# Kernel optimization log

Hardware: AMD Instinct MI355X
Metric: run time of the kernel (lower is better)

Reference implementation:

```python
import jax, jax.numpy as jnp
import numpy as np

DIM = 256
CDIM = 512
HEADS = 8
DIM_HEAD = 32
HID = HEADS * DIM_HEAD          # 256
MLP_DIM = int(DIM * 2.5)        # 640
B, T, TC = 8, 8192, 8192
GROUPS = 32
EPS = 1e-5


def setup_inputs() -> dict:
    key = jax.random.key(0)
    ks = jax.random.split(key, 12)
    w = lambda k, shape: jax.random.normal(k, shape, jnp.float32) * 0.02
    return {
        "x": jax.random.normal(ks[0], (B, DIM, T), jnp.float32),
        "c": jax.random.normal(ks[1], (B, CDIM, TC), jnp.float32),
        # self-attn (LinearAttention)
        "W_qkv": w(ks[2], (3 * HID, DIM)),
        "W_so": w(ks[3], (DIM, HID)), "b_so": jnp.zeros((DIM,), jnp.float32),
        "sa_g": jnp.ones((DIM,), jnp.float32), "sa_b": jnp.zeros((DIM,), jnp.float32),
        # cross-attn (LinearAttentionC)
        "W_cq": w(ks[4], (HID, DIM)),
        "W_ckv": w(ks[5], (2 * HID, CDIM)),
        "W_co": w(ks[6], (DIM, HID)), "b_co": jnp.zeros((DIM,), jnp.float32),
        "ca_g": jnp.ones((DIM,), jnp.float32), "ca_b": jnp.zeros((DIM,), jnp.float32),
        # MLP
        "W_m1": w(ks[7], (MLP_DIM, DIM)), "b_m1": jnp.zeros((MLP_DIM,), jnp.float32),
        "W_m2": w(ks[8], (DIM, MLP_DIM)), "b_m2": jnp.zeros((DIM,), jnp.float32),
        # pre-norms
        "nm_g": jnp.ones((DIM,), jnp.float32), "nm_b": jnp.zeros((DIM,), jnp.float32),
        "nm1_g": jnp.ones((DIM,), jnp.float32), "nm1_b": jnp.zeros((DIM,), jnp.float32),
        "nm2_g": jnp.ones((DIM,), jnp.float32), "nm2_b": jnp.zeros((DIM,), jnp.float32),
        "nm3_g": jnp.ones((CDIM,), jnp.float32), "nm3_b": jnp.zeros((CDIM,), jnp.float32),
    }


def group_norm(x, g, b):
    Bx, C, Tx = x.shape
    xg = x.reshape(Bx, GROUPS, C // GROUPS, Tx)
    mu = xg.mean(axis=(2, 3), keepdims=True)
    var = ((xg - mu) ** 2).mean(axis=(2, 3), keepdims=True)
    xn = ((xg - mu) * jax.lax.rsqrt(var + EPS)).reshape(Bx, C, Tx)
    return xn * g[None, :, None] + b[None, :, None]


def conv1(x, W, b=None):
    # 1x1 Conv1d == channel matmul: W [out, in], x [b, in, t]
    y = jnp.einsum('oc,bct->bot', W, x)
    return y if b is None else y + b[None, :, None]


def split_heads(t):
    Bx, HC, Tx = t.shape
    return t.reshape(Bx, HEADS, HC // HEADS, Tx)  # b h c t


def linear_attention(q, k, v):
    # q,k,v: [b, h, d, t]
    scale = DIM_HEAD ** -0.5
    q = jax.nn.softmax(q, axis=-2) * scale   # softmax over feature dim d
    k = jax.nn.softmax(k, axis=-1)           # softmax over time t
    ctx = jnp.einsum('bhdn,bhen->bhde', k, v)   # [b,h,d,e] tiny per-head context
    out = jnp.einsum('bhde,bhdn->bhen', ctx, q)
    Bx, H, E, Tx = out.shape
    return out.reshape(Bx, H * E, Tx)  # b (h c) t


def reference(x, c, W_qkv, W_so, b_so, sa_g, sa_b,
              W_cq, W_ckv, W_co, b_co, ca_g, ca_b,
              W_m1, b_m1, W_m2, b_m2,
              nm_g, nm_b, nm1_g, nm1_b, nm2_g, nm2_b, nm3_g, nm3_b):
    # --- self linear attention + residual ---
    h = group_norm(x, nm_g, nm_b)
    q, k, v = map(split_heads, jnp.split(conv1(h, W_qkv), 3, axis=1))
    o = linear_attention(q, k, v)
    o = group_norm(conv1(o, W_so, b_so), sa_g, sa_b)
    x = o + x
    # --- cross linear attention + residual ---
    h = group_norm(x, nm1_g, nm1_b)
    cn = group_norm(c, nm3_g, nm3_b)
    q = split_heads(conv1(h, W_cq))
    k, v = map(split_heads, jnp.split(conv1(cn, W_ckv), 2, axis=1))
    o = linear_attention(q, k, v)
    o = group_norm(conv1(o, W_co, b_co), ca_g, ca_b)
    x = o + x
    # --- SiLU MLP + residual ---
    h = group_norm(x, nm2_g, nm2_b)
    h = jax.nn.silu(conv1(h, W_m1, b_m1))
    x = conv1(h, W_m2, b_m2) + x
    return x
```

## Files before the change

kernel.cpp:

```cpp
#include <hip/hip_runtime.h>
#include <cmath>

typedef unsigned short u16;
typedef __attribute__((ext_vector_type(8))) __bf16 bf16x8;
typedef __attribute__((ext_vector_type(4))) float f32x4;

#define DEV static __device__ __forceinline__

DEV float b2f(u16 u){ union{unsigned i; float f;} v; v.i=((unsigned)u)<<16; return v.f; }
DEV u16 f2b(float f){ union{float f; unsigned i;} v; v.f=f; unsigned r = v.i + 0x7FFFu + ((v.i>>16)&1u); return (u16)(r>>16); }

#define GLL(g,l) __builtin_amdgcn_global_load_lds((const __attribute__((address_space(1))) void*)(g), (__attribute__((address_space(3))) void*)(l), 16, 0, 0)

__global__ void k_init(const float* __restrict__ s0,const float* __restrict__ s1,
                       const float* __restrict__ s2, u16* __restrict__ d,
                       float* __restrict__ stats){
  const int bid = blockIdx.x;
  if (bid == 1152){
    #pragma unroll
    for (int j=0;j<12;j++){ const int idx=j*256+threadIdx.x; if (idx<3072) stats[idx]=0.f; }
    return;
  }
  const int i = bid*256 + threadIdx.x;
  const float* s; int off;
  if      (i < 65536){ s=s0; off=0; }
  else if (i < 131072){ s=s1; off=65536; }
  else                { s=s2; off=131072; }
  d[i] = f2b(s[i-off]);
}

DEV void fold_body(const float* W, const float* g, const float* beta, const float* base,
                   const float* stats, u16* Wb, float* biasb, int O, int K, int chsh,
                   float inv_n, int o, int b){
  const int tid = threadIdx.x;
  float bp = 0.f;
  for (int k = tid; k < K; k += 256){
    const int gr = k >> chsh;
    const float s = stats[(b*32+gr)*2], s2 = stats[(b*32+gr)*2+1];
    const float mu = s*inv_n;
    const float rs = rsqrtf(s2*inv_n - mu*mu + 1e-5f);
    const float w = W[(long)o*K + k];
    const float gg = g[k]*rs;
    Wb[((long)b*O + o)*K + k] = f2b(w*gg);
    bp += w*(beta[k] - mu*gg);
  }
  __shared__ float red[256];
  red[tid] = bp; __syncthreads();
  for (int off=128; off>0; off>>=1){ if (tid<off) red[tid]+=red[tid+off]; __syncthreads(); }
  if (tid==0) biasb[b*O+o] = red[0] + (base ? base[o] : 0.f);
}

__global__ void k_fold(const float* __restrict__ W, const float* __restrict__ g,
                       const float* __restrict__ beta, const float* __restrict__ base,
                       const float* __restrict__ stats, u16* __restrict__ Wb,
                       float* __restrict__ biasb, int O, int K, int chsh, float inv_n){
  fold_body(W,g,beta,base,stats,Wb,biasb,O,K,chsh,inv_n,blockIdx.x,blockIdx.y);
}

__global__ void k_fold2(const float* __restrict__ W1, const float* __restrict__ g1,
                        const float* __restrict__ be1, const float* __restrict__ st1,
                        u16* __restrict__ Wb1, float* __restrict__ bb1, int O1, int K1, int chsh1, float inv1,
                        const float* __restrict__ W2, const float* __restrict__ g2,
                        const float* __restrict__ be2, const float* __restrict__ st2,
                        u16* __restrict__ Wb2, float* __restrict__ bb2, int O2, int K2, int chsh2, float inv2){
  const int o = blockIdx.x, b = blockIdx.y;
  if (o < O1) fold_body(W1,g1,be1,nullptr,st1,Wb1,bb1,O1,K1,chsh1,inv1,o,b);
  else        fold_body(W2,g2,be2,nullptr,st2,Wb2,bb2,O2,K2,chsh2,inv2,o-O1,b);
}

__global__ void k_transs(const float* __restrict__ xsrc, const float* __restrict__ csrc,
                         u16* __restrict__ xdst, u16* __restrict__ cdst,
                         float* __restrict__ xstat, float* __restrict__ cstat){
  const int b = blockIdx.z;
  const int gy = blockIdx.y;
  const float* src; u16* dst; float* stat; int C, chsh, c0;
  if (gy < 4){ src=xsrc; dst=xdst; stat=xstat; C=256; chsh=3; c0=gy*64; }
  else       { src=csrc; dst=cdst; stat=cstat; C=512; chsh=4; c0=(gy-4)*64; }
  const int t0 = blockIdx.x*64;
  const int tid = threadIdx.x;
  __shared__ float tile[64][65];
  __shared__ float grp[16];
  if (tid < 16) grp[tid] = 0.f;
  float s_acc[4], s2_acc[4];
  #pragma unroll
  for (int p=0;p<4;p++){
    const int cc = (tid>>4) + p*16, tt = (tid&15)*4;
    const float4 v = *(const float4*)&src[((long)b*C + c0+cc)*8192 + t0+tt];
    tile[cc][tt+0]=v.x; tile[cc][tt+1]=v.y; tile[cc][tt+2]=v.z; tile[cc][tt+3]=v.w;
    s_acc[p]  = v.x+v.y+v.z+v.w;
    s2_acc[p] = v.x*v.x+v.y*v.y+v.z*v.z+v.w*v.w;
  }
  __syncthreads();
  #pragma unroll
  for (int p=0;p<4;p++){
    float s = s_acc[p], s2 = s2_acc[p];
    #pragma unroll
    for (int m=1; m<16; m<<=1){ s += __shfl_xor(s, m); s2 += __shfl_xor(s2, m); }
    if ((tid&15)==0){
      const int gl = ((tid>>4) + p*16) >> chsh;
      atomicAdd(&grp[gl*2],   s);
      atomicAdd(&grp[gl*2+1], s2);
    }
  }
  #pragma unroll
  for (int p=0;p<4;p++){
    const int tt = (tid>>4) + p*16, c4 = (tid&15)*4;
    u16 rbi[4];
    #pragma unroll
    for (int j=0;j<4;j++) rbi[j] = f2b(tile[c4+j][tt]);
    ushort4 rv; rv.x=rbi[0]; rv.y=rbi[1]; rv.z=rbi[2]; rv.w=rbi[3];
    *(ushort4*)&dst[((long)b*8192 + t0+tt)*C + c0+c4] = rv;
  }
  __syncthreads();
  const int ngr = 64>>chsh;
  if (tid < ngr*2){
    atomicAdd(&stat[((b*32) + (c0>>chsh))*2 + tid], grp[tid]);
  }
}

template<bool OUTB, bool BIAS, bool SILU, bool RES, bool STATS, bool SPLIT, bool TRANS>
__global__ __launch_bounds__(256,2) void k_gemm(
    const u16* __restrict__ A, const u16* __restrict__ W,
    float* __restrict__ outF, u16* __restrict__ outB,
    const float* __restrict__ bias, const u16* __restrict__ res,
    float* __restrict__ stat, int K, int O, long wsb, int bsb)
{
  __shared__ u16 As[128*64];
  __shared__ u16 Ws[128*64];
  __shared__ float sb[128][2];
  const int tid = threadIdx.x;
  const int wv = tid>>6, lane = tid&63;
  const int nwg = (int)(gridDim.x*gridDim.y);
  int fid = (int)(blockIdx.y*gridDim.x + blockIdx.x);
  fid = (fid&7)*(nwg>>3) + (fid>>3);
  const long t0 = (long)(fid / (int)gridDim.x)*128;
  const int o0 = (fid % (int)gridDim.x)*128;
  const int bb = (int)(t0>>13);
  const u16* Wp = W + (long)bb*wsb;
  const int wt = (wv>>1)*64, wo = (wv&1)*64;
  const int lr = lane>>3, lc = (lane&7)*8;
  f32x4 acc[4][4] = {};
  for (int kc = 0; kc < K; kc += 64){
    #pragma unroll
    for (int it = 0; it < 4; ++it){
      const int r = wv*32 + it*8;
      GLL(A + (t0 + r + lr)*(long)K + kc + lc, &As[r*64]);
      GLL(Wp + (long)(o0 + r + lr)*K + kc + lc, &Ws[r*64]);
    }
    __syncthreads();
    #pragma unroll
    for (int ks=0; ks<2; ++ks){
      const int kb = ks*32 + (lane>>4)*8;
      bf16x8 af[4], bfr[4];
      #pragma unroll
      for (int i=0;i<4;i++) af[i]  = *(const bf16x8*)&As[(wt + i*16 + (lane&15))*64 + kb];
      #pragma unroll
      for (int j=0;j<4;j++) bfr[j] = *(const bf16x8*)&Ws[(wo + j*16 + (lane&15))*64 + kb];
      #pragma unroll
      for (int i=0;i<4;i++)
        #pragma unroll
        for (int j=0;j<4;j++)
          acc[i][j] = __builtin_amdgcn_mfma_f32_16x16x32_bf16(af[i], bfr[j], acc[i][j], 0, 0, 0);
    }
    __syncthreads();
  }
  if (STATS){
    if (tid < 128){ sb[tid][0]=0.f; sb[tid][1]=0.f; }
    __syncthreads();
  }
  const int q = lane>>4, cc = lane&15;
  #pragma unroll
  for (int j=0;j<4;j++){
    const int o = o0 + wo + j*16 + cc;
    const float bv = BIAS ? bias[bsb*bb + o] : 0.f;
    float ts=0.f, ts2=0.f;
    #pragma unroll
    for (int i=0;i<4;i++){
      const long tb = t0 + wt + i*16 + q*4;
      if (TRANS){
        float vv[4];
        #pragma unroll
        for (int r=0;r<4;r++){
          float v = acc[i][j][r] + bv;
          if (SILU) v = v * (1.f/(1.f + __expf(-v)));
          if (RES) v += b2f(res[(tb + r)*(long)O + o]);
          vv[r] = v;
        }
        float4 v4; v4.x=vv[0]; v4.y=vv[1]; v4.z=vv[2]; v4.w=vv[3];
        *(float4*)&outF[(((tb>>13)*(long)O + o)<<13) + (tb&8191)] = v4;
      } else {
        #pragma unroll
        for (int r=0;r<4;r++){
          float v = acc[i][j][r] + bv;
          if (SILU) v = v * (1.f/(1.f + __expf(-v)));
          long idx;
          if (SPLIT) idx = ((long)(o>>8)<<24) + (tb + r)*256 + (o&255);
          else       idx = (tb + r)*(long)O + o;
          if (RES) v += b2f(res[idx]);
          if (STATS){ ts += v; ts2 += v*v; }
          if (OUTB) outB[idx] = f2b(v); else outF[idx] = v;
        }
      }
    }
    if (STATS){
      const int ol = wo + j*16 + cc;
      atomicAdd(&sb[ol][0], ts);
      atomicAdd(&sb[ol][1], ts2);
    }
  }
  if (STATS){
    __syncthreads();
    if (tid < 16){
      float u=0.f, u2=0.f;
      #pragma unroll
      for (int j2=0;j2<8;j2++){ u += sb[tid*8+j2][0]; u2 += sb[tid*8+j2][1]; }
      atomicAdd(&stat[(bb*32 + (o0>>3) + tid)*2],   u);
      atomicAdd(&stat[(bb*32 + (o0>>3) + tid)*2+1], u2);
    }
  }
}

__global__ __launch_bounds__(256,2) void k_ctx(const u16* __restrict__ kp, const u16* __restrict__ vp,
                                               float* __restrict__ part){
  const int tid = threadIdx.x;
  const int b = blockIdx.x >> 6, seg = blockIdx.x & 63;
  const int h = tid>>5, d = tid&31;
  __shared__ u16 kb[16][256];
  __shared__ float vf[16][260];
  float acc[32];
  #pragma unroll
  for (int e=0;e<32;e++) acc[e]=0.f;
  float ks = 0.f;
  const long rb = (long)b*8192 + seg*128;
  const int w = tid>>6, sub = tid&63;
  for (int tc=0; tc<128; tc+=16){
    #pragma unroll
    for (int p=0;p<4;p++){
      const int row = p*4 + w;
      const long rowbase = (rb + tc + row)*256;
      if (sub < 32){
        uint4 val = *(const uint4*)(kp + rowbase + sub*8);
        *(uint4*)&kb[row][sub*8] = val;
      } else {
        const int s2 = sub-32;
        uint4 val = *(const uint4*)(vp + rowbase + s2*8);
        const u16* vs = (const u16*)&val;
        float4 f0 = {b2f(vs[0]),b2f(vs[1]),b2f(vs[2]),b2f(vs[3])};
        float4 f1 = {b2f(vs[4]),b2f(vs[5]),b2f(vs[6]),b2f(vs[7])};
        *(float4*)&vf[row][s2*8] = f0;
        *(float4*)&vf[row][s2*8+4] = f1;
      }
    }
    __syncthreads();
    #pragma unroll
    for (int r=0;r<16;r++){
      const float kpv = __expf(b2f(kb[r][h*32+d]));
      ks += kpv;
      #pragma unroll
      for (int e4=0;e4<8;e4++){
        const float4 v4 = *(const float4*)&vf[r][h*32+e4*4];
        acc[e4*4+0] += kpv*v4.x; acc[e4*4+1] += kpv*v4.y;
        acc[e4*4+2] += kpv*v4.z; acc[e4*4+3] += kpv*v4.w;
      }
    }
    __syncthreads();
  }
  float* pb = part + (long)blockIdx.x*8448;
  #pragma unroll
  for (int e=0;e<32;e++) pb[e*256 + tid] = acc[e];
  pb[8192 + tid] = ks;
}

__global__ void k_ctxred(const float* __restrict__ part, float* __restrict__ ctx,
                         float* __restrict__ ksumF){
  if (blockIdx.x >= 256){
    const int j = (blockIdx.x-256)*256 + threadIdx.x;
    #pragma unroll
    for (int q=0;q<4;q++){
      const int idx = j*4+q;
      const int b = idx>>8, cch = idx&255;
      float s=0.f;
      for (int g=0; g<64; g++) s += part[((long)(b*64+g))*8448 + 8192 + cch];
      ksumF[idx] = s;
    }
    return;
  }
  const int i = blockIdx.x*256 + threadIdx.x;
  const int b = i>>13, r = i&8191;
  float s=0.f;
  for (int g=0; g<64; g++) s += part[((long)(b*64+g))*8448 + r];
  ctx[i] = s;
}

__global__ void k_attnout(const u16* __restrict__ q, const float* __restrict__ ctx,
                          const float* __restrict__ ksumF, u16* __restrict__ out){
  const int b = blockIdx.x >> 8, t0 = (blockIdx.x & 255)*32;
  __shared__ float cs[8512];
  for (int i=threadIdx.x; i<8192; i+=256){
    const int e=i>>8, cch=i&255;
    cs[(cch>>5)*1064 + (cch&31)*33 + e] = ctx[(b<<13) + i] / ksumF[b*256 + cch];
  }
  __syncthreads();
  const int t = t0 + (threadIdx.x>>3), h = threadIdx.x&7;
  const u16* qp = q + ((long)b*8192 + t)*256 + h*32;
  uint4 qv[4];
  #pragma unroll
  for (int j=0;j<4;j++) qv[j] = ((const uint4*)qp)[j];
  const u16* qs = (const u16*)qv;
  float qe[32]; float ssum = 0.f;
  #pragma unroll
  for (int dd=0; dd<32; dd++){ qe[dd] = __expf(b2f(qs[dd])); ssum += qe[dd]; }
  const float inv = 0.17677669529663687f / ssum;
  float o[32];
  #pragma unroll
  for (int e=0;e<32;e++) o[e]=0.f;
  const float* ch = &cs[h*1064];
  #pragma unroll
  for (int dd=0; dd<32; dd++){
    const float w = qe[dd]*inv;
    #pragma unroll
    for (int e=0;e<32;e++) o[e] += w * ch[dd*33+e];
  }
  u16 ob[32];
  #pragma unroll
  for (int e=0;e<32;e++) ob[e] = f2b(o[e]);
  uint4* op = (uint4*)(out + ((long)b*8192 + t)*256 + h*32);
  const uint4* obv = (const uint4*)ob;
  #pragma unroll
  for (int j=0;j<4;j++) op[j] = obv[j];
}

__global__ void k_gnres(const u16* __restrict__ conv, u16* __restrict__ xr,
                        const float* __restrict__ sums_in, float* __restrict__ sums_out,
                        const float* __restrict__ g, const float* __restrict__ bt){
  const int blk = blockIdx.x;
  const int b = blk>>7;
  const long base = (long)blk*4096;
  const int tid = threadIdx.x;
  const int c0 = (tid<<2)&255;
  const int gr = c0>>3;
  const float s = sums_in[(b*32+gr)*2], s2 = sums_in[(b*32+gr)*2+1];
  const float mu = s*(1.f/65536.f);
  const float rs = rsqrtf(s2*(1.f/65536.f) - mu*mu + 1e-5f);
  float gg[4], bb[4];
  #pragma unroll
  for (int j=0;j<4;j++){ gg[j] = g[c0+j]*rs; bb[j] = bt[c0+j] - mu*gg[j]; }
  float ts=0.f, ts2=0.f;
  for (int it=0; it<16; ++it){
    const long i4 = base + it*256 + tid;
    ushort4 cv = ((const ushort4*)conv)[i4];
    ushort4 rv = ((const ushort4*)xr)[i4];
    float ov[4];
    const float ci[4] = {b2f(cv.x),b2f(cv.y),b2f(cv.z),b2f(cv.w)};
    const float ri[4] = {b2f(rv.x),b2f(rv.y),b2f(rv.z),b2f(rv.w)};
    #pragma unroll
    for (int j=0;j<4;j++){
      ov[j] = ci[j]*gg[j] + bb[j] + ri[j];
      ts += ov[j]; ts2 += ov[j]*ov[j];
    }
    ushort4 o4; o4.x=f2b(ov[0]); o4.y=f2b(ov[1]); o4.z=f2b(ov[2]); o4.w=f2b(ov[3]);
    ((ushort4*)xr)[i4] = o4;
  }
  __shared__ float grp[32][2];
  if (tid<32){ grp[tid][0]=0.f; grp[tid][1]=0.f; }
  __syncthreads();
  atomicAdd(&grp[gr][0], ts);
  atomicAdd(&grp[gr][1], ts2);
  __syncthreads();
  if (tid<32){
    atomicAdd(&sums_out[(b*32+tid)*2],   grp[tid][0]);
    atomicAdd(&sums_out[(b*32+tid)*2+1], grp[tid][1]);
  }
}

extern "C" void kernel_launch(void* const* d_in, const int* in_sizes, int n_in,
                              void* d_out, int out_size, void* d_ws, size_t ws_size,
                              hipStream_t stream){
  (void)in_sizes; (void)n_in; (void)out_size; (void)ws_size;
  const float* x   = (const float*)d_in[0];
  const float* c   = (const float*)d_in[1];
  const float* W_qkv=(const float*)d_in[2];
  const float* W_so =(const float*)d_in[3];
  const float* b_so =(const float*)d_in[4];
  const float* sa_g =(const float*)d_in[5];
  const float* sa_b =(const float*)d_in[6];
  const float* W_cq =(const float*)d_in[7];
  const float* W_ckv=(const float*)d_in[8];
  const float* W_co =(const float*)d_in[9];
  const float* b_co =(const float*)d_in[10];
  const float* ca_g =(const float*)d_in[11];
  const float* ca_b =(const float*)d_in[12];
  const float* W_m1 =(const float*)d_in[13];
  const float* b_m1 =(const float*)d_in[14];
  const float* W_m2 =(const float*)d_in[15];
  const float* b_m2 =(const float*)d_in[16];
  const float* nm_g =(const float*)d_in[17];
  const float* nm_b =(const float*)d_in[18];
  const float* nm1_g=(const float*)d_in[19];
  const float* nm1_b=(const float*)d_in[20];
  const float* nm2_g=(const float*)d_in[21];
  const float* nm2_b=(const float*)d_in[22];
  const float* nm3_g=(const float*)d_in[23];
  const float* nm3_b=(const float*)d_in[24];
  float* out = (float*)d_out;

  char* ws = (char*)d_ws;
  const size_t MB = 1024ull*1024ull;
  u16* wSO = (u16*)ws;
  u16* wCO = wSO + 65536;
  u16* wM2 = wCO + 65536;
  float* stats = (float*)(ws + 1*MB);
  float* xstat = stats;
  float* cstat = stats + 512;
  float* so_sum= stats + 1024;
  float* x1_sum= stats + 1536;
  float* co_sum= stats + 2048;
  float* x2_sum= stats + 2560;
  float* ksumF = stats + 3072;
  float* ctxb  = stats + 8192;
  float* bQKV = (float*)(ws + 2*MB);
  float* bCKV = bQKV + 6144;
  float* bCQ  = bCKV + 4096;
  float* bM1  = bCQ + 2048;
  u16* wQKVb = (u16*)(ws + 3*MB);
  u16* wCKVb = (u16*)(ws + 6*MB);
  u16* wCQb  = (u16*)(ws + 10*MB);
  u16* wM1b  = (u16*)(ws + 11*MB);
  u16*   xT    = (u16*)(ws + 16*MB);
  u16*   cT    = (u16*)(ws + 48*MB);
  float* part  = (float*)(ws + 112*MB);
  u16*   qkvb  = (u16*)(ws + 136*MB);
  u16*   kvb   = (u16*)(ws + 232*MB);
  u16*   convb = kvb;
  u16*   attno = (u16*)(ws + 296*MB);
  const long SEG = 1L<<24;

  k_init<<<1153,256,0,stream>>>(W_so, W_co, W_m2, wSO, stats);

  k_transs<<<dim3(128,12,8),256,0,stream>>>(x, c, xT, cT, xstat, cstat);

  k_fold2<<<dim3(1280,8),256,0,stream>>>(W_qkv, nm_g, nm_b, xstat, wQKVb, bQKV, 768, 256, 3, 1.f/65536.f,
                                         W_ckv, nm3_g, nm3_b, cstat, wCKVb, bCKV, 512, 512, 4, 1.f/131072.f);
  k_gemm<true,true,false,false,false,true,false><<<dim3(6,512),256,0,stream>>>(xT, wQKVb, nullptr, qkvb, bQKV, nullptr, nullptr, 256, 768, 196608, 768);
  k_ctx<<<512,256,0,stream>>>(qkvb+SEG, qkvb+2*SEG, part);
  k_ctxred<<<258,256,0,stream>>>(part, ctxb, ksumF);
  k_attnout<<<2048,256,0,stream>>>(qkvb, ctxb, ksumF, attno);
  k_gemm<true,true,false,false,true,false,false><<<dim3(2,512),256,0,stream>>>(attno, wSO, nullptr, convb, b_so, nullptr, so_sum, 256, 256, 0, 0);
  k_gnres<<<1024,256,0,stream>>>(convb, xT, so_sum, x1_sum, sa_g, sa_b);

  k_fold<<<dim3(256,8),256,0,stream>>>(W_cq, nm1_g, nm1_b, nullptr, x1_sum, wCQb, bCQ, 256, 256, 3, 1.f/65536.f);
  k_gemm<true,true,false,false,false,false,false><<<dim3(2,512),256,0,stream>>>(xT, wCQb, nullptr, qkvb, bCQ, nullptr, nullptr, 256, 256, 65536, 256);
  k_gemm<true,true,false,false,false,true,false><<<dim3(4,512),256,0,stream>>>(cT, wCKVb, nullptr, kvb, bCKV, nullptr, nullptr, 512, 512, 262144, 512);
  k_ctx<<<512,256,0,stream>>>(kvb, kvb+SEG, part);
  k_ctxred<<<258,256,0,stream>>>(part, ctxb, ksumF);
  k_attnout<<<2048,256,0,stream>>>(qkvb, ctxb, ksumF, attno);
  k_gemm<true,true,false,false,true,false,false><<<dim3(2,512),256,0,stream>>>(attno, wCO, nullptr, convb, b_co, nullptr, co_sum, 256, 256, 0, 0);
  k_gnres<<<1024,256,0,stream>>>(convb, xT, co_sum, x2_sum, ca_g, ca_b);

  k_fold<<<dim3(640,8),256,0,stream>>>(W_m1, nm2_g, nm2_b, b_m1, x2_sum, wM1b, bM1, 640, 256, 3, 1.f/65536.f);
  k_gemm<true,true,true,false,false,false,false><<<dim3(5,512),256,0,stream>>>(xT, wM1b, nullptr, qkvb, bM1, nullptr, nullptr, 256, 640, 163840, 640);
  k_gemm<false,true,false,true,false,false,true><<<dim3(2,512),256,0,stream>>>(qkvb, wM2, out, nullptr, b_m2, xT, nullptr, 640, 256, 0, 0);
}
```

Baseline: 873.4 us.

## Widen transpose-and-stats tiles to 256 channels with bf16 swizzled LDS

```diff
diff --git a/kernel.cpp b/kernel.cpp
--- a/kernel.cpp
+++ b/kernel.cpp
@@ -68,53 +68,62 @@
   else        fold_body(W2,g2,be2,nullptr,st2,Wb2,bb2,O2,K2,chsh2,inv2,o-O1,b);
 }
 
-__global__ void k_transs(const float* __restrict__ xsrc, const float* __restrict__ csrc,
-                         u16* __restrict__ xdst, u16* __restrict__ cdst,
-                         float* __restrict__ xstat, float* __restrict__ cstat){
-  const int b = blockIdx.z;
-  const int gy = blockIdx.y;
-  const float* src; u16* dst; float* stat; int C, chsh, c0;
-  if (gy < 4){ src=xsrc; dst=xdst; stat=xstat; C=256; chsh=3; c0=gy*64; }
-  else       { src=csrc; dst=cdst; stat=cstat; C=512; chsh=4; c0=(gy-4)*64; }
-  const int t0 = blockIdx.x*64;
+__global__ __launch_bounds__(256) void k_trf(const float* __restrict__ xsrc, const float* __restrict__ csrc,
+                                             u16* __restrict__ xdst, u16* __restrict__ cdst,
+                                             float* __restrict__ xstat, float* __restrict__ cstat){
+  __shared__ u16 tile[64*264];
+  __shared__ float grp[64];
   const int tid = threadIdx.x;
-  __shared__ float tile[64][65];
-  __shared__ float grp[16];
-  if (tid < 16) grp[tid] = 0.f;
-  float s_acc[4], s2_acc[4];
-  #pragma unroll
-  for (int p=0;p<4;p++){
-    const int cc = (tid>>4) + p*16, tt = (tid&15)*4;
-    const float4 v = *(const float4*)&src[((long)b*C + c0+cc)*8192 + t0+tt];
-    tile[cc][tt+0]=v.x; tile[cc][tt+1]=v.y; tile[cc][tt+2]=v.z; tile[cc][tt+3]=v.w;
-    s_acc[p]  = v.x+v.y+v.z+v.w;
-    s2_acc[p] = v.x*v.x+v.y*v.y+v.z*v.z+v.w*v.w;
+  const int bid = blockIdx.x;
+  const float* src; u16* dst; float* stat; int C, chsh, b, t0, c0;
+  if (bid < 1024){ src=xsrc; dst=xdst; stat=xstat; C=256; chsh=3;
+    b = bid>>7; t0 = (bid&127)*64; c0 = 0; }
+  else { const int r2 = bid-1024; src=csrc; dst=cdst; stat=cstat; C=512; chsh=4;
+    b = r2>>8; const int r = r2&255; t0 = (r>>1)*64; c0 = (r&1)*256; }
+  if (tid < 64) grp[tid] = 0.f;
+  const int ccb = tid>>4;
+  const int ttl = (tid&15)*4;
+  const long sbase = ((long)b*C + c0 + ccb)*8192 + t0 + ttl;
+  float4 v[16];
+  #pragma unroll
+  for (int p=0;p<16;p++)
+    v[p] = *(const float4*)&src[sbase + (long)p*16*8192];
+  float sred[16], s2red[16];
+  #pragma unroll
+  for (int p=0;p<16;p++){
+    const int cc = ccb + p*16;
+    #pragma unroll
+    for (int j=0;j<4;j++){
+      const int row = ttl + j;
+      const float fv = (j==0)?v[p].x:(j==1)?v[p].y:(j==2)?v[p].z:v[p].w;
+      tile[row*264 + (cc ^ ((row&15)<<4))] = f2b(fv);
+    }
+    float s = v[p].x+v[p].y+v[p].z+v[p].w;
+    float s2 = v[p].x*v[p].x+v[p].y*v[p].y+v[p].z*v[p].z+v[p].w*v[p].w;
+    #pragma unroll
+    for (int m=1;m<16;m<<=1){ s += __shfl_xor(s,m); s2 += __shfl_xor(s2,m); }
+    sred[p]=s; s2red[p]=s2;
   }
   __syncthreads();
-  #pragma unroll
-  for (int p=0;p<4;p++){
-    float s = s_acc[p], s2 = s2_acc[p];
-    #pragma unroll
-    for (int m=1; m<16; m<<=1){ s += __shfl_xor(s, m); s2 += __shfl_xor(s2, m); }
-    if ((tid&15)==0){
-      const int gl = ((tid>>4) + p*16) >> chsh;
-      atomicAdd(&grp[gl*2],   s);
-      atomicAdd(&grp[gl*2+1], s2);
-    }
-  }
-  #pragma unroll
-  for (int p=0;p<4;p++){
-    const int tt = (tid>>4) + p*16, c4 = (tid&15)*4;
-    u16 rbi[4];
-    #pragma unroll
-    for (int j=0;j<4;j++) rbi[j] = f2b(tile[c4+j][tt]);
-    ushort4 rv; rv.x=rbi[0]; rv.y=rbi[1]; rv.z=rbi[2]; rv.w=rbi[3];
-    *(ushort4*)&dst[((long)b*8192 + t0+tt)*C + c0+c4] = rv;
+  const int wv = tid>>6, lane = tid&63;
+  #pragma unroll
+  for (int q=0;q<16;q++){
+    const int tt = q*4 + wv;
+    const ushort4 o = *(const ushort4*)&tile[tt*264 + ((lane*4) ^ ((tt&15)<<4))];
+    *(ushort4*)&dst[((long)b*8192 + t0 + tt)*C + c0 + lane*4] = o;
+  }
+  if ((tid&15)==0){
+    #pragma unroll
+    for (int p=0;p<16;p++){
+      const int gl = (ccb + p*16)>>chsh;
+      atomicAdd(&grp[gl*2],   sred[p]);
+      atomicAdd(&grp[gl*2+1], s2red[p]);
+    }
   }
   __syncthreads();
-  const int ngr = 64>>chsh;
-  if (tid < ngr*2){
-    atomicAdd(&stat[((b*32) + (c0>>chsh))*2 + tid], grp[tid]);
+  const int ngr2 = (256>>chsh)*2;
+  if (tid < ngr2){
+    atomicAdd(&stat[(b*32 + (c0>>chsh))*2 + tid], grp[tid]);
   }
 }
 
@@ -437,7 +446,7 @@
 
   k_init<<<1153,256,0,stream>>>(W_so, W_co, W_m2, wSO, stats);
 
-  k_transs<<<dim3(128,12,8),256,0,stream>>>(x, c, xT, cT, xstat, cstat);
+  k_trf<<<3072,256,0,stream>>>(x, c, xT, cT, xstat, cstat);
 
   k_fold2<<<dim3(1280,8),256,0,stream>>>(W_qkv, nm_g, nm_b, xstat, wQKVb, bQKV, 768, 256, 3, 1.f/65536.f,
                                          W_ckv, nm3_g, nm3_b, cstat, wCKVb, bCKV, 512, 512, 4, 1.f/131072.f);
```

Result: no change. 876.7 us (+0.4%).
